# Kernel optimization log

Hardware: AMD Instinct MI355X
Metric: run time of the kernel (lower is better)

The kernel has to match this reference:

```python
import jax, jax.numpy as jnp
import numpy as np

# ---- exact Hungarian (Jonker-Volgenant / e-maxx shortest augmenting path) ----

def _lsa(cost):
    """Square cost matrix [n,n] (numpy) -> col index assigned to each row (optimal)."""
    n = cost.shape[0]
    a = np.zeros((n + 1, n + 1), dtype=np.float64)
    a[1:, 1:] = cost
    u = np.zeros(n + 1)
    v = np.zeros(n + 1)
    p = np.zeros(n + 1, dtype=np.int64)   # p[j] = row matched to column j (1-indexed)
    way = np.zeros(n + 1, dtype=np.int64)
    for i in range(1, n + 1):
        p[0] = i
        j0 = 0
        minv = np.full(n + 1, np.inf)
        used = np.zeros(n + 1, dtype=bool)
        while True:
            used[j0] = True
            i0 = p[j0]
            cur = a[i0] - u[i0] - v
            better = (~used) & (cur < minv)
            minv[better] = cur[better]
            way[better] = j0
            masked = np.where(used, np.inf, minv)
            j1 = int(np.argmin(masked))
            delta = masked[j1]
            u[p[used]] += delta
            v[used] -= delta
            minv[~used] -= delta
            j0 = j1
            if p[j0] == 0:
                break
        while j0 != 0:
            j1 = way[j0]
            p[j0] = p[j1]
            j0 = j1
    col = np.zeros(n, dtype=np.int64)
    for j in range(1, n + 1):
        col[p[j] - 1] = j - 1
    return col


def _lsa_batch(costs):
    """costs [..., N, N] numpy -> assigned col per row [..., N]."""
    N = costs.shape[-1]
    flat = costs.reshape(-1, N, N)
    cols = np.stack([_lsa(c) for c in flat])
    return cols.reshape(costs.shape[:-1])


# ---- kernel pieces (same math as cdist_torch / material_distances) ----

def _pair_sqdist(v1, v2):
    g = jnp.einsum('pnd,bmd->pbnm', v1, v2)
    s1 = (v1 ** 2).sum(-1)
    s2 = (v2 ** 2).sum(-1)
    return jnp.abs(-2.0 * g + s1[:, None, :, None] + s2[None, :, None, :])


def _self_sqdist(v):
    # v [B,N,d] -> [B,N,N]; only diagonal pairs of Material_kernel(x,x) are needed
    g = jnp.einsum('bnd,bmd->bnm', v, v)
    s = (v ** 2).sum(-1)
    return jnp.abs(-2.0 * g + s[:, :, None] + s[:, None, :])


def _material_kernel(D2, cols):
    # sum_i exp(-D2[..., i, cols[..., i]]) / N  (Hungarian-matched similarity)
    sel = jnp.take_along_axis(D2, cols[..., None], axis=-1)[..., 0]
    return jnp.exp(-sel).sum(-1) / D2.shape[-1]


def setup_inputs():
    key = jax.random.key(0)
    ks = jax.random.split(key, 4)
    P, B, A, d = 64, 32, 40, 128
    x = jax.random.normal(ks[0], (B, A, d), jnp.float32)
    data_points = jax.random.normal(ks[1], (P, A, d), jnp.float32)
    gamma = jnp.full((1, d), -2.0, jnp.float32)  # matches __init__: ones(1,n_in)*-2
    M = jax.random.normal(ks[2], (P, P), jnp.float32)
    K = M @ M.T + P * jnp.eye(P, dtype=jnp.float32)
    L = jnp.linalg.cholesky(K).astype(jnp.float32)  # valid trained-state Cholesky buffer
    alpha = jax.random.normal(ks[3], (P,), jnp.float32)
    return {"x": x, "data_points": data_points, "gamma": gamma, "L": L, "alpha": alpha}


def reference(x, data_points, gamma, L, alpha):
    g = jnp.exp(gamma)                      # [1,d]
    v1 = data_points * g                    # [P,A,d]
    v2 = x * g                              # [B,A,d]
    D2 = _pair_sqdist(v1, v2)               # [P,B,A,A]
    cols = jnp.asarray(_lsa_batch(np.asarray(D2, np.float64)))
    K_xnew = _material_kernel(D2, cols)     # [P,B]
    Linv = jnp.linalg.inv(L)
    v = Linv @ K_xnew                       # [P,B]
    mean = jnp.einsum('in,i->n', K_xnew, alpha)
    Ds = _self_sqdist(v2)                   # [B,A,A] (diagonal of K(x,x) only)
    cols_s = jnp.asarray(_lsa_batch(np.asarray(Ds, np.float64)))
    kxx = _material_kernel(Ds, cols_s)      # [B]
    var = kxx - jnp.einsum('in,in->n', v, v)
    return mean, var
```

## Files before the change

### kernel.cpp

```cpp
#include <hip/hip_runtime.h>
#include <math.h>

#define P_N 64
#define B_N 32
#define A_N 40
#define D_N 128

__device__ __forceinline__ int readlane_i(int v, int l) {
  return __builtin_amdgcn_readlane(v, l);
}
__device__ __forceinline__ float readlane_f(float v, int l) {
  return __int_as_float(__builtin_amdgcn_readlane(__float_as_int(v), l));
}
__device__ __forceinline__ unsigned ordf(float f) {
  unsigned b = __float_as_uint(f);
  return b ^ (((unsigned)((int)b >> 31)) | 0x80000000u);
}
__device__ __forceinline__ unsigned wave_min_u32(unsigned x) {
  unsigned t;
  t = (unsigned)__builtin_amdgcn_update_dpp((int)0xFFFFFFFFu, (int)x, 0x111, 0xF, 0xF, false);
  x = t < x ? t : x;
  t = (unsigned)__builtin_amdgcn_update_dpp((int)0xFFFFFFFFu, (int)x, 0x112, 0xF, 0xF, false);
  x = t < x ? t : x;
  t = (unsigned)__builtin_amdgcn_update_dpp((int)0xFFFFFFFFu, (int)x, 0x114, 0xF, 0xF, false);
  x = t < x ? t : x;
  t = (unsigned)__builtin_amdgcn_update_dpp((int)0xFFFFFFFFu, (int)x, 0x118, 0xF, 0xF, false);
  x = t < x ? t : x;
  t = (unsigned)__builtin_amdgcn_update_dpp((int)0xFFFFFFFFu, (int)x, 0x142, 0xA, 0xF, false);
  x = t < x ? t : x;
  t = (unsigned)__builtin_amdgcn_update_dpp((int)0xFFFFFFFFu, (int)x, 0x143, 0xC, 0xF, false);
  x = t < x ? t : x;
  return (unsigned)__builtin_amdgcn_readlane((int)x, 63);
}

__global__ __launch_bounds__(64) void hungarian_pair(
    const float* __restrict__ DP, const float* __restrict__ X,
    const float* __restrict__ G, float* __restrict__ out) {
  __shared__ float Cs[A_N * A_N];
  __shared__ float g_lds[D_N];
  const int bid  = blockIdx.x;
  const int lane = threadIdx.x;
  const float* __restrict__ Abase = DP + (bid >> 5) * (A_N * D_N);
  const float* __restrict__ Bbase = X  + (bid & 31) * (A_N * D_N);

  g_lds[lane]      = expf(G[lane]);
  g_lds[lane + 64] = expf(G[lane + 64]);
  __syncthreads();

  if (lane < A_N) {
    const float* bp = Bbase + lane * D_N;
    for (int c = 0; c < 4; ++c) {
      float4 gg[8], bb[8];
      #pragma unroll
      for (int k = 0; k < 8; ++k) {
        gg[k] = ((const float4*)(g_lds + c * 32))[k];
        float4 br = ((const float4*)(bp + c * 32))[k];
        bb[k] = make_float4(br.x * gg[k].x, br.y * gg[k].y,
                            br.z * gg[k].z, br.w * gg[k].w);
      }
      for (int i = 0; i < A_N; ++i) {
        const float4* ap = (const float4*)(Abase + i * D_N + c * 32);
        float s = 0.f;
        #pragma unroll
        for (int k = 0; k < 8; ++k) {
          float4 a = ap[k];
          float dx = fmaf(a.x, gg[k].x, -bb[k].x); s = fmaf(dx, dx, s);
          float dy = fmaf(a.y, gg[k].y, -bb[k].y); s = fmaf(dy, dy, s);
          float dz = fmaf(a.z, gg[k].z, -bb[k].z); s = fmaf(dz, dz, s);
          float dw = fmaf(a.w, gg[k].w, -bb[k].w); s = fmaf(dw, dw, s);
        }
        if (c == 0) Cs[i * A_N + lane] = s;
        else        Cs[i * A_N + lane] += s;
      }
    }
  }
  __syncthreads();

  const int  cix     = (lane >= 1 && lane <= A_N) ? (lane - 1) : 0;
  const bool realcol = (lane >= 1 && lane <= A_N);

  float vpot = 0.f;
  int   amin = 0;
  if (realcol) {
    float mn = INFINITY; int mi = 0;
    for (int i = 0; i < A_N; ++i) {
      float c = Cs[i * A_N + cix];
      if (c < mn) { mn = c; mi = i; }
    }
    vpot = mn; amin = mi + 1;
  }

  unsigned long long rmask = 0ull;
  int p = 0, way = 0;
  for (int j = 1; j <= A_N; ++j) {
    int am = readlane_i(amin, j);
    if (!((rmask >> am) & 1ull)) {
      rmask |= 1ull << am;
      if (lane == j) p = am;
    }
  }

  float u = 0.f;

  for (int i = 1; i <= A_N; ++i) {
    if ((rmask >> i) & 1ull) continue;
    float r = realcol ? (Cs[(i - 1) * A_N + cix] - vpot) : INFINITY;
    unsigned key = (ordf(r) & 0xFFFFFFC0u) | (unsigned)lane;
    unsigned kmin = wave_min_u32(key);
    int jm = (int)(kmin & 63u);
    int pj = readlane_i(p, jm);
    if (pj == 0) {
      float rmin = readlane_f(r, jm);
      if (lane == jm) p = i;
      if (lane == i)  u = rmin;
      rmask |= 1ull << i;
    }
  }

  for (int f = 1; f <= A_N; ++f) {
    if ((rmask >> f) & 1ull) continue;
    if (lane == 0) p = f;
    float mhat = INFINITY;
    float excl = realcol ? 0.f : INFINITY;
    float dsum = 0.f;
    float dent = 0.f, rent = 0.f;
    bool  used   = !realcol;
    bool  intree = (lane == f);
    int   j0 = 0, i0 = f;
    const unsigned plane_key = ((unsigned)p << 6) | (unsigned)lane;
    for (int guard = 0; guard < 42; ++guard) {
      float Craw = Cs[(i0 - 1) * A_N + cix];
      float uc   = readlane_f(u, i0);
      float off  = dsum - uc - vpot + excl;
      float cand = Craw + off;
      if (cand < mhat) way = j0;
      mhat = fminf(mhat, cand);
      unsigned key = (ordf(mhat) & 0xFFFFF000u) | plane_key;
      unsigned kmin = wave_min_u32(key);
      int j1 = (int)(kmin & 63u);
      int i1 = (int)((kmin >> 6) & 63u);
      float dnew = readlane_f(mhat, j1);
      if (lane == j1) { used = true; dent = dnew; excl = INFINITY; mhat = INFINITY; }
      dsum = dnew;
      j0 = j1;
      i0 = i1;
      if (i1 == 0) break;
      if (lane == i1) { intree = true; rent = dnew; }
    }
    if (used && realcol) vpot -= (dsum - dent);
    if (intree)          u    += (dsum - rent);
    while (j0 != 0) {
      int jn = readlane_i(way, j0);
      int pn = readlane_i(p, jn);
      if (lane == j0) p = pn;
      j0 = jn;
    }
  }

  float e = 0.f;
  if (realcol) e = expf(-Cs[(p - 1) * A_N + (lane - 1)]);
  #pragma unroll
  for (int off = 32; off; off >>= 1) e += __shfl_xor(e, off);
  if (lane == 0) out[bid] = e / 40.0f;
}

__global__ __launch_bounds__(64) void final_kernel(
    const float* __restrict__ Kx, const float* __restrict__ L,
    const float* __restrict__ alpha, float* __restrict__ out) {
  int b = threadIdx.x;
  if (b >= B_N) return;
  float mean = 0.f;
  #pragma unroll
  for (int p = 0; p < P_N; ++p) mean = fmaf(Kx[p * B_N + b], alpha[p], mean);
  out[b] = mean;
  float vr[P_N];
  float sumv2 = 0.f;
  #pragma unroll
  for (int i = 0; i < P_N; ++i) {
    float s = Kx[i * B_N + b];
    #pragma unroll
    for (int j = 0; j < i; ++j) s = fmaf(-L[i * P_N + j], vr[j], s);
    float vi = s / L[i * P_N + i];
    vr[i] = vi;
    sumv2 = fmaf(vi, vi, sumv2);
  }
  out[B_N + b] = 1.0f - sumv2;
}

extern "C" void kernel_launch(void* const* d_in, const int* in_sizes, int n_in,
                              void* d_out, int out_size, void* d_ws, size_t ws_size,
                              hipStream_t stream) {
  const float* x     = (const float*)d_in[0];
  const float* dp    = (const float*)d_in[1];
  const float* gamma = (const float*)d_in[2];
  const float* L     = (const float*)d_in[3];
  const float* alpha = (const float*)d_in[4];
  float* out = (float*)d_out;

  float* Kx = (float*)d_ws;

  hungarian_pair<<<P_N * B_N, 64, 0, stream>>>(dp, x, gamma, Kx);
  final_kernel<<<1, 64, 0, stream>>>(Kx, L, alpha, out);
}
```

Baseline: 129.5 us.

## Keep per-lane cost column in registers instead of LDS for Hungarian loops

Each lane now keeps its 40-entry cost-matrix column in named registers instead of a shared-memory matrix. Rows are picked with a uniform switch plus a small select tree, so the serial augmenting-path loop no longer waits on LDS reads, and the block barrier after the distance phase is gone. The reduced minimum is now decoded straight from the wave-min key rather than fetched with a readlane. That decoded value has its low mantissa bits truncated, which slightly perturbs the dual potentials. The change raises register pressure, with launch bounds asking for two waves per SIMD.

```diff
diff --git a/kernel.cpp b/kernel.cpp
--- a/kernel.cpp
+++ b/kernel.cpp
@@ -16,6 +16,10 @@
   unsigned b = __float_as_uint(f);
   return b ^ (((unsigned)((int)b >> 31)) | 0x80000000u);
 }
+__device__ __forceinline__ float unordf(unsigned k) {
+  unsigned b = k ^ (((unsigned)((int)(~k) >> 31)) | 0x80000000u);
+  return __uint_as_float(b);
+}
 __device__ __forceinline__ unsigned wave_min_u32(unsigned x) {
   unsigned t;
   t = (unsigned)__builtin_amdgcn_update_dpp((int)0xFFFFFFFFu, (int)x, 0x111, 0xF, 0xF, false);
@@ -33,13 +37,62 @@
   return (unsigned)__builtin_amdgcn_readlane((int)x, 63);
 }
 
-__global__ __launch_bounds__(64) void hungarian_pair(
+__device__ __forceinline__ float mux8(float r0, float r1, float r2, float r3,
+                                      float r4, float r5, float r6, float r7, int k) {
+  float a = (k & 1) ? r1 : r0;
+  float b = (k & 1) ? r3 : r2;
+  float c = (k & 1) ? r5 : r4;
+  float d = (k & 1) ? r7 : r6;
+  float e = (k & 2) ? b : a;
+  float f = (k & 2) ? d : c;
+  return (k & 4) ? f : e;
+}
+
+#define R40(M) M(0) M(1) M(2) M(3) M(4) M(5) M(6) M(7) M(8) M(9) \
+  M(10) M(11) M(12) M(13) M(14) M(15) M(16) M(17) M(18) M(19) \
+  M(20) M(21) M(22) M(23) M(24) M(25) M(26) M(27) M(28) M(29) \
+  M(30) M(31) M(32) M(33) M(34) M(35) M(36) M(37) M(38) M(39)
+
+#define SEL40U(dst, kk) do { int _q = (kk); int _k = _q & 7;                     \
+  switch (_q >> 3) {                                                             \
+    case 0:  dst = mux8(c0,  c1,  c2,  c3,  c4,  c5,  c6,  c7,  _k); break;      \
+    case 1:  dst = mux8(c8,  c9,  c10, c11, c12, c13, c14, c15, _k); break;      \
+    case 2:  dst = mux8(c16, c17, c18, c19, c20, c21, c22, c23, _k); break;      \
+    case 3:  dst = mux8(c24, c25, c26, c27, c28, c29, c30, c31, _k); break;      \
+    default: dst = mux8(c32, c33, c34, c35, c36, c37, c38, c39, _k); break; }    \
+  } while (0)
+
+#define SEL40D(dst, kk) do { int _q = (kk); int _k = _q & 7; int _g = _q >> 3;   \
+  float _m0 = mux8(c0,  c1,  c2,  c3,  c4,  c5,  c6,  c7,  _k);                  \
+  float _m1 = mux8(c8,  c9,  c10, c11, c12, c13, c14, c15, _k);                  \
+  float _m2 = mux8(c16, c17, c18, c19, c20, c21, c22, c23, _k);                  \
+  float _m3 = mux8(c24, c25, c26, c27, c28, c29, c30, c31, _k);                  \
+  float _m4 = mux8(c32, c33, c34, c35, c36, c37, c38, c39, _k);                  \
+  float _a = (_g & 1) ? _m1 : _m0; float _b = (_g & 1) ? _m3 : _m2;              \
+  _a = (_g & 2) ? _b : _a; dst = (_g & 4) ? _m4 : _a; } while (0)
+
+__device__ __forceinline__ float chunk_dist(const float4* __restrict__ ap,
+                                            const float4 (&gg)[8], const float4 (&bb)[8]) {
+  float s = 0.f;
+  #pragma unroll
+  for (int k = 0; k < 8; ++k) {
+    float4 a = ap[k];
+    float dx = fmaf(a.x, gg[k].x, -bb[k].x); s = fmaf(dx, dx, s);
+    float dy = fmaf(a.y, gg[k].y, -bb[k].y); s = fmaf(dy, dy, s);
+    float dz = fmaf(a.z, gg[k].z, -bb[k].z); s = fmaf(dz, dz, s);
+    float dw = fmaf(a.w, gg[k].w, -bb[k].w); s = fmaf(dw, dw, s);
+  }
+  return s;
+}
+
+__global__ __launch_bounds__(64, 2) void hungarian_pair(
     const float* __restrict__ DP, const float* __restrict__ X,
     const float* __restrict__ G, float* __restrict__ out) {
-  __shared__ float Cs[A_N * A_N];
   __shared__ float g_lds[D_N];
   const int bid  = blockIdx.x;
   const int lane = threadIdx.x;
+  const bool realcol = (lane >= 1 && lane <= A_N);
+  const int  cix     = realcol ? (lane - 1) : 0;
   const float* __restrict__ Abase = DP + (bid >> 5) * (A_N * D_N);
   const float* __restrict__ Bbase = X  + (bid & 31) * (A_N * D_N);
 
@@ -47,8 +100,12 @@
   g_lds[lane + 64] = expf(G[lane + 64]);
   __syncthreads();
 
-  if (lane < A_N) {
-    const float* bp = Bbase + lane * D_N;
+#define C_DECL(n) float c##n = 0.f;
+  R40(C_DECL)
+#undef C_DECL
+
+  if (realcol) {
+    const float* bp = Bbase + cix * D_N;
     for (int c = 0; c < 4; ++c) {
       float4 gg[8], bb[8];
       #pragma unroll
@@ -58,35 +115,19 @@
         bb[k] = make_float4(br.x * gg[k].x, br.y * gg[k].y,
                             br.z * gg[k].z, br.w * gg[k].w);
       }
-      for (int i = 0; i < A_N; ++i) {
-        const float4* ap = (const float4*)(Abase + i * D_N + c * 32);
-        float s = 0.f;
-        #pragma unroll
-        for (int k = 0; k < 8; ++k) {
-          float4 a = ap[k];
-          float dx = fmaf(a.x, gg[k].x, -bb[k].x); s = fmaf(dx, dx, s);
-          float dy = fmaf(a.y, gg[k].y, -bb[k].y); s = fmaf(dy, dy, s);
-          float dz = fmaf(a.z, gg[k].z, -bb[k].z); s = fmaf(dz, dz, s);
-          float dw = fmaf(a.w, gg[k].w, -bb[k].w); s = fmaf(dw, dw, s);
-        }
-        if (c == 0) Cs[i * A_N + lane] = s;
-        else        Cs[i * A_N + lane] += s;
-      }
-    }
-  }
-  __syncthreads();
-
-  const int  cix     = (lane >= 1 && lane <= A_N) ? (lane - 1) : 0;
-  const bool realcol = (lane >= 1 && lane <= A_N);
+#define BROW(n) c##n += chunk_dist((const float4*)(Abase + n * D_N + c * 32), gg, bb);
+      R40(BROW)
+#undef BROW
+    }
+  }
 
   float vpot = 0.f;
   int   amin = 0;
   if (realcol) {
-    float mn = INFINITY; int mi = 0;
-    for (int i = 0; i < A_N; ++i) {
-      float c = Cs[i * A_N + cix];
-      if (c < mn) { mn = c; mi = i; }
-    }
+    float mn = c0; int mi = 0;
+#define CMIN(n) if (c##n < mn) { mn = c##n; mi = n; }
+    R40(CMIN)
+#undef CMIN
     vpot = mn; amin = mi + 1;
   }
 
@@ -104,7 +145,8 @@
 
   for (int i = 1; i <= A_N; ++i) {
     if ((rmask >> i) & 1ull) continue;
-    float r = realcol ? (Cs[(i - 1) * A_N + cix] - vpot) : INFINITY;
+    float r = INFINITY;
+    if (realcol) { float cv; SEL40U(cv, i - 1); r = cv - vpot; }
     unsigned key = (ordf(r) & 0xFFFFFFC0u) | (unsigned)lane;
     unsigned kmin = wave_min_u32(key);
     int jm = (int)(kmin & 63u);
@@ -129,7 +171,7 @@
     int   j0 = 0, i0 = f;
     const unsigned plane_key = ((unsigned)p << 6) | (unsigned)lane;
     for (int guard = 0; guard < 42; ++guard) {
-      float Craw = Cs[(i0 - 1) * A_N + cix];
+      float Craw; SEL40U(Craw, i0 - 1);
       float uc   = readlane_f(u, i0);
       float off  = dsum - uc - vpot + excl;
       float cand = Craw + off;
@@ -139,7 +181,7 @@
       unsigned kmin = wave_min_u32(key);
       int j1 = (int)(kmin & 63u);
       int i1 = (int)((kmin >> 6) & 63u);
-      float dnew = readlane_f(mhat, j1);
+      float dnew = unordf(kmin & 0xFFFFF000u);
       if (lane == j1) { used = true; dent = dnew; excl = INFINITY; mhat = INFINITY; }
       dsum = dnew;
       j0 = j1;
@@ -157,8 +199,9 @@
     }
   }
 
-  float e = 0.f;
-  if (realcol) e = expf(-Cs[(p - 1) * A_N + (lane - 1)]);
+  int pk = realcol ? (p - 1) : 0;
+  float cm; SEL40D(cm, pk);
+  float e = realcol ? expf(-cm) : 0.f;
   #pragma unroll
   for (int off = 32; off; off >>= 1) e += __shfl_xor(e, off);
   if (lane == 0) out[bid] = e / 40.0f;
```

Measured after the change: 152.9 us. 1.18x slower.

## Add JV augmenting row reduction with top-2 wave min before Hungarian augmentation

Applied to the files above, without the earlier changes.

Replaces the simple greedy row-assignment pass with a Jonker-Volgenant style augmenting row reduction. It uses a new DPP wave reduction that returns the smallest and second-smallest keys, so it can lower column potentials and displace earlier assignments. The aim is to leave fewer free rows for the costly shortest-augmenting-path phase. It also recovers dnew by decoding the truncated min key instead of doing a readlane, which trades some precision in the potentials for one fewer dependent read. The extra reduction work per ARR step and the 12-bit key truncation could change tie-breaking and accuracy.

```diff
diff --git a/kernel.cpp b/kernel.cpp
--- a/kernel.cpp
+++ b/kernel.cpp
@@ -16,6 +16,10 @@
   unsigned b = __float_as_uint(f);
   return b ^ (((unsigned)((int)b >> 31)) | 0x80000000u);
 }
+__device__ __forceinline__ float unordf(unsigned k) {
+  unsigned b = k ^ (((unsigned)((int)(~k) >> 31)) | 0x80000000u);
+  return __uint_as_float(b);
+}
 __device__ __forceinline__ unsigned wave_min_u32(unsigned x) {
   unsigned t;
   t = (unsigned)__builtin_amdgcn_update_dpp((int)0xFFFFFFFFu, (int)x, 0x111, 0xF, 0xF, false);
@@ -31,6 +35,24 @@
   t = (unsigned)__builtin_amdgcn_update_dpp((int)0xFFFFFFFFu, (int)x, 0x143, 0xC, 0xF, false);
   x = t < x ? t : x;
   return (unsigned)__builtin_amdgcn_readlane((int)x, 63);
+}
+__device__ __forceinline__ void wave_min2_u32(unsigned x, unsigned &m1o, unsigned &m2o) {
+  unsigned m1 = x, m2 = 0xFFFFFFFFu;
+  unsigned t1, t2, lo, hi;
+#define MIN2_STAGE(ctrl, rm) \
+  t1 = (unsigned)__builtin_amdgcn_update_dpp((int)0xFFFFFFFFu, (int)m1, ctrl, rm, 0xF, false); \
+  t2 = (unsigned)__builtin_amdgcn_update_dpp((int)0xFFFFFFFFu, (int)m2, ctrl, rm, 0xF, false); \
+  lo = m1 < t1 ? m1 : t1; hi = m1 < t1 ? t1 : m1;                                              \
+  m2 = m2 < t2 ? m2 : t2; m2 = m2 < hi ? m2 : hi; m1 = lo;
+  MIN2_STAGE(0x111, 0xF)
+  MIN2_STAGE(0x112, 0xF)
+  MIN2_STAGE(0x114, 0xF)
+  MIN2_STAGE(0x118, 0xF)
+  MIN2_STAGE(0x142, 0xA)
+  MIN2_STAGE(0x143, 0xC)
+#undef MIN2_STAGE
+  m1o = (unsigned)__builtin_amdgcn_readlane((int)m1, 63);
+  m2o = (unsigned)__builtin_amdgcn_readlane((int)m2, 63);
 }
 
 __global__ __launch_bounds__(64) void hungarian_pair(
@@ -102,23 +124,43 @@
 
   float u = 0.f;
 
-  for (int i = 1; i <= A_N; ++i) {
-    if ((rmask >> i) & 1ull) continue;
-    float r = realcol ? (Cs[(i - 1) * A_N + cix] - vpot) : INFINITY;
-    unsigned key = (ordf(r) & 0xFFFFFFC0u) | (unsigned)lane;
-    unsigned kmin = wave_min_u32(key);
-    int jm = (int)(kmin & 63u);
-    int pj = readlane_i(p, jm);
-    if (pj == 0) {
-      float rmin = readlane_f(r, jm);
-      if (lane == jm) p = i;
-      if (lane == i)  u = rmin;
-      rmask |= 1ull << i;
-    }
-  }
-
-  for (int f = 1; f <= A_N; ++f) {
-    if ((rmask >> f) & 1ull) continue;
+  unsigned long long fmask = (((1ull << (A_N + 1)) - 2ull)) & ~rmask;
+  unsigned long long dmask = 0ull;
+  {
+    int I = 0; bool chaining = false; int iters = 0;
+    while ((chaining || fmask) && iters < 64) {
+      if (!chaining) { I = __builtin_ctzll(fmask); fmask &= fmask - 1ull; }
+      ++iters;
+      float r = realcol ? (Cs[(I - 1) * A_N + cix] - vpot) : INFINITY;
+      unsigned key = (ordf(r) & 0xFFFFFFC0u) | (unsigned)lane;
+      unsigned m1, m2;
+      wave_min2_u32(key, m1, m2);
+      int   j1  = (int)(m1 & 63u);
+      float u1  = readlane_f(r, j1);
+      float u2a = unordf(m2 & 0xFFFFFFC0u);
+      int   k   = readlane_i(p, j1);
+      bool  strict = (u1 < u2a);
+      if (strict || k == 0) {
+        if (strict) {
+          if (lane == j1) vpot -= (u2a - u1);
+          if (lane == I)  u = u2a;
+        } else {
+          if (lane == I)  u = u1;
+        }
+        if (lane == j1) p = I;
+        if (k != 0) { I = k; chaining = true; }
+        else        chaining = false;
+      } else {
+        dmask |= 1ull << I;
+        chaining = false;
+      }
+    }
+    if (chaining) dmask |= 1ull << I;
+    dmask |= fmask;
+  }
+
+  while (dmask) {
+    int f = __builtin_ctzll(dmask); dmask &= dmask - 1ull;
     if (lane == 0) p = f;
     float mhat = INFINITY;
     float excl = realcol ? 0.f : INFINITY;
@@ -139,7 +181,7 @@
       unsigned kmin = wave_min_u32(key);
       int j1 = (int)(kmin & 63u);
       int i1 = (int)((kmin >> 6) & 63u);
-      float dnew = readlane_f(mhat, j1);
+      float dnew = unordf(kmin & 0xFFFFF000u);
       if (lane == j1) { used = true; dent = dnew; excl = INFINITY; mhat = INFINITY; }
       dsum = dnew;
       j0 = j1;
```

After: 127.7 us (median of 2 runs). About the same (-1.4%).
